# Performance work log

Hardware: AMD Instinct MI355X
Metric: run time of the kernel (lower is better)

Reference implementation:

```python
import jax, jax.numpy as jnp
import numpy as np

N = 100000   # nodes
E = 1600000  # edges
D = 64       # feature dim (input = hidden = output)
G = 256      # graphs in batch
EPS = 1e-5   # BatchNorm eps


def setup_inputs() -> dict:
    key = jax.random.key(0)
    ks = jax.random.split(key, 16)
    inp = {
        "x": jax.random.normal(ks[0], (N, D), dtype=jnp.float32),
        "edge_index": jax.random.randint(ks[1], (2, E), 0, N, dtype=jnp.int64),
        "batch": jnp.sort(jax.random.randint(ks[2], (N,), 0, G, dtype=jnp.int64)),
    }
    # GCNConv weights (glorot-ish) + biases, and BatchNorm affine params, 3 layers
    for i in range(3):
        inp[f"W{i+1}"] = jax.random.normal(ks[3 + i], (D, D), dtype=jnp.float32) / np.sqrt(D)
        inp[f"b{i+1}"] = jnp.zeros((D,), dtype=jnp.float32)
        inp[f"g{i+1}"] = jnp.ones((D,), dtype=jnp.float32)   # BN gamma
        inp[f"be{i+1}"] = jnp.zeros((D,), dtype=jnp.float32)  # BN beta
    return inp


def _batchnorm(x, gamma, beta):
    # BatchNorm1d in training mode: batch stats over the node dim (biased var)
    mean = jnp.mean(x, axis=0)
    var = jnp.mean(jnp.square(x - mean), axis=0)
    return (x - mean) * jax.lax.rsqrt(var + EPS) * gamma + beta


def reference(x, edge_index, batch, W1, b1, g1, be1, W2, b2, g2, be2, W3, b3, g3, be3):
    src, dst = edge_index[0], edge_index[1]
    # GCN normalization with self-loops: norm_ij = deg_i^-1/2 * deg_j^-1/2 over A + I
    loop = jnp.arange(N, dtype=src.dtype)
    src2 = jnp.concatenate([src, loop])
    dst2 = jnp.concatenate([dst, loop])
    deg = jax.ops.segment_sum(jnp.ones_like(src2, dtype=x.dtype), dst2, num_segments=N)
    dinv = jax.lax.rsqrt(deg)  # deg >= 1 thanks to self loops
    norm = (dinv[src2] * dinv[dst2])[:, None]  # [E+N, 1]

    def gcn_conv(h, W, b):
        h = h @ W                                   # [N, D] small GEMM
        msg = h[src2] * norm                        # per-edge gather (memory bound)
        return jax.ops.segment_sum(msg, dst2, num_segments=N) + b

    params = [(W1, b1, g1, be1), (W2, b2, g2, be2), (W3, b3, g3, be3)]
    h = x
    for i, (W, b, g, be) in enumerate(params):
        h = gcn_conv(h, W, b)
        h = _batchnorm(h, g, be)
        if i < 2:
            h = jax.nn.relu(h)
            # dropout(p=0.2) is identity in deterministic/eval reference

    # global mean + max pool per graph
    ones = jnp.ones((N,), dtype=h.dtype)
    cnt = jax.ops.segment_sum(ones, batch, num_segments=G)            # [G]
    s = jax.ops.segment_sum(h, batch, num_segments=G)                 # [G, D]
    mean = s / jnp.maximum(cnt, 1.0)[:, None]
    mx = jax.ops.segment_max(h, batch, num_segments=G)
    mx = jnp.where(cnt[:, None] > 0, mx, 0.0)
    return mean + mx
```

## Files before the change

kernel.cpp:

```cpp
#include <hip/hip_runtime.h>
#include <hip/hip_bf16.h>
#include <math.h>

#define N_NODES 100000
#define N_EDGES 1600000
#define DIM 64
#define N_GRAPHS 256
#define BN_EPS 1e-5f
#define N_XCD 8
#define BUCKET ((N_NODES + N_XCD - 1) / N_XCD)
#define FILL_CHUNKS 128
#define FILL_ESIZE ((N_EDGES + FILL_CHUNKS - 1) / FILL_CHUNKS)
#define CSR_STRIDE 48

__device__ inline unsigned short f2bf(float f) {
    __hip_bfloat16 h = __float2bfloat16(f);
    return *reinterpret_cast<unsigned short*>(&h);
}
__device__ inline unsigned int pack2bf(float a, float b) {
    return (unsigned int)f2bf(a) | ((unsigned int)f2bf(b) << 16);
}
__device__ inline float bf_lo(unsigned int u) { return __uint_as_float(u << 16); }
__device__ inline float bf_hi(unsigned int u) { return __uint_as_float(u & 0xffff0000u); }

__global__ __launch_bounds__(256) void hist_fused(const int* __restrict__ src,
                                                  const int* __restrict__ dst,
                                                  int* __restrict__ cnt,
                                                  int* __restrict__ csr_pad) {
    int chunk = blockIdx.x >> 3;
    int lo = (blockIdx.x & (N_XCD - 1)) * BUCKET;
    int e0 = chunk * FILL_ESIZE;
    int e1 = min(e0 + FILL_ESIZE, N_EDGES);
    for (int e = e0 + threadIdx.x; e < e1; e += 256) {
        int d = __builtin_nontemporal_load(&dst[e]);
        if ((unsigned)(d - lo) < (unsigned)BUCKET) {
            int r = atomicAdd(&cnt[d], 1);
            csr_pad[d * CSR_STRIDE + r] = __builtin_nontemporal_load(&src[e]);
        }
    }
}

__global__ void deg_fin(const int* __restrict__ cnt, float* __restrict__ dinv) {
    int i = blockIdx.x * blockDim.x + threadIdx.x;
    if (i < N_NODES) dinv[i] = rsqrtf((float)(cnt[i] + 1));
}

__global__ __launch_bounds__(256) void gemm_f32(const float* __restrict__ h,
                                                const float* __restrict__ W,
                                                const float* __restrict__ dinv,
                                                unsigned short* __restrict__ tb) {
    int tid = threadIdx.x;
    int d = tid & 63;
    int wv = tid >> 6;
    float wcol[64];
    #pragma unroll
    for (int k = 0; k < 64; ++k) wcol[k] = W[k * 64 + d];
    int nwaves = gridDim.x * 4;
    for (int row = blockIdx.x * 4 + wv; row < N_NODES; row += nwaves) {
        int urow = __builtin_amdgcn_readfirstlane(row);
        const float* hr = h + (size_t)urow * 64;
        float a0 = 0.f, a1 = 0.f, a2 = 0.f, a3 = 0.f;
        #pragma unroll
        for (int k = 0; k < 64; k += 4) {
            a0 = fmaf(hr[k + 0], wcol[k + 0], a0);
            a1 = fmaf(hr[k + 1], wcol[k + 1], a1);
            a2 = fmaf(hr[k + 2], wcol[k + 2], a2);
            a3 = fmaf(hr[k + 3], wcol[k + 3], a3);
        }
        float acc = (a0 + a1) + (a2 + a3);
        tb[(size_t)urow * 64 + d] = f2bf(acc * dinv[urow]);
    }
}

__global__ __launch_bounds__(256) void bnrelu(const unsigned short* __restrict__ agg,
                                              const float* __restrict__ stats,
                                              const float* __restrict__ gamma,
                                              const float* __restrict__ beta,
                                              float* __restrict__ hp) {
    __shared__ float scale[64], shift[64];
    int tid = threadIdx.x;
    if (tid < 64) {
        const float inv_n = 1.0f / (float)N_NODES;
        float mean = stats[tid] * inv_n;
        float var = fmaxf(stats[64 + tid] * inv_n - mean * mean, 0.f);
        float rs = rsqrtf(var + BN_EPS) * gamma[tid];
        scale[tid] = rs;
        shift[tid] = beta[tid] - mean * rs;
    }
    __syncthreads();
    const size_t total = (size_t)N_NODES * 8;
    for (size_t i = (size_t)blockIdx.x * 256 + tid; i < total; i += (size_t)gridDim.x * 256) {
        uint4 u = *reinterpret_cast<const uint4*>(agg + i * 8);
        int dd = (int)((i * 8) & 63);
        float4 o0, o1;
        o0.x = fmaxf(fmaf(bf_lo(u.x), scale[dd + 0], shift[dd + 0]), 0.f);
        o0.y = fmaxf(fmaf(bf_hi(u.x), scale[dd + 1], shift[dd + 1]), 0.f);
        o0.z = fmaxf(fmaf(bf_lo(u.y), scale[dd + 2], shift[dd + 2]), 0.f);
        o0.w = fmaxf(fmaf(bf_hi(u.y), scale[dd + 3], shift[dd + 3]), 0.f);
        o1.x = fmaxf(fmaf(bf_lo(u.z), scale[dd + 4], shift[dd + 4]), 0.f);
        o1.y = fmaxf(fmaf(bf_hi(u.z), scale[dd + 5], shift[dd + 5]), 0.f);
        o1.z = fmaxf(fmaf(bf_lo(u.w), scale[dd + 6], shift[dd + 6]), 0.f);
        o1.w = fmaxf(fmaf(bf_hi(u.w), scale[dd + 7], shift[dd + 7]), 0.f);
        *reinterpret_cast<float4*>(hp + i * 8) = o0;
        *reinterpret_cast<float4*>(hp + i * 8 + 4) = o1;
    }
}

__global__ __launch_bounds__(256) void gather_agg(const int* __restrict__ csr_pad,
                                                  const int* __restrict__ cnt,
                                                  const float* __restrict__ dinv,
                                                  const unsigned short* __restrict__ tb,
                                                  const float* __restrict__ bias,
                                                  unsigned short* __restrict__ out,
                                                  float* __restrict__ stats) {
    int tid = threadIdx.x;
    int wave = tid >> 6;
    int lane = tid & 63;
    int q    = lane >> 4;
    int ql   = lane & 15;

    float4 s4  = {0.f, 0.f, 0.f, 0.f};
    float4 sq4 = {0.f, 0.f, 0.f, 0.f};

    for (int v = blockIdx.x * 4 + wave; v < N_NODES; v += gridDim.x * 4) {
        int beg = v * CSR_STRIDE;
        int end = beg + cnt[v];
        float4 acc  = {0.f, 0.f, 0.f, 0.f};
        float4 acc2 = {0.f, 0.f, 0.f, 0.f};
        int e = beg + q;
        for (; e + 4 < end; e += 8) {
            int s0 = csr_pad[e];
            int s1 = csr_pad[e + 4];
            uint2 u0 = *reinterpret_cast<const uint2*>(tb + (size_t)s0 * 64 + ql * 4);
            uint2 u1 = *reinterpret_cast<const uint2*>(tb + (size_t)s1 * 64 + ql * 4);
            acc.x  += bf_lo(u0.x); acc.y  += bf_hi(u0.x);
            acc.z  += bf_lo(u0.y); acc.w  += bf_hi(u0.y);
            acc2.x += bf_lo(u1.x); acc2.y += bf_hi(u1.x);
            acc2.z += bf_lo(u1.y); acc2.w += bf_hi(u1.y);
        }
        if (e < end) {
            int s0 = csr_pad[e];
            uint2 u0 = *reinterpret_cast<const uint2*>(tb + (size_t)s0 * 64 + ql * 4);
            acc.x += bf_lo(u0.x); acc.y += bf_hi(u0.x);
            acc.z += bf_lo(u0.y); acc.w += bf_hi(u0.y);
        }
        acc.x += acc2.x; acc.y += acc2.y; acc.z += acc2.z; acc.w += acc2.w;

        acc.x += __shfl_xor(acc.x, 16, 64); acc.x += __shfl_xor(acc.x, 32, 64);
        acc.y += __shfl_xor(acc.y, 16, 64); acc.y += __shfl_xor(acc.y, 32, 64);
        acc.z += __shfl_xor(acc.z, 16, 64); acc.z += __shfl_xor(acc.z, 32, 64);
        acc.w += __shfl_xor(acc.w, 16, 64); acc.w += __shfl_xor(acc.w, 32, 64);

        if (q == 0) {
            float di = dinv[v];
            uint2 uv = *reinterpret_cast<const uint2*>(tb + (size_t)v * 64 + ql * 4);
            float4 bi = *reinterpret_cast<const float4*>(bias + ql * 4);
            float4 val;
            val.x = fmaf(di, acc.x + bf_lo(uv.x), bi.x);
            val.y = fmaf(di, acc.y + bf_hi(uv.x), bi.y);
            val.z = fmaf(di, acc.z + bf_lo(uv.y), bi.z);
            val.w = fmaf(di, acc.w + bf_hi(uv.y), bi.w);
            uint2 o;
            o.x = pack2bf(val.x, val.y);
            o.y = pack2bf(val.z, val.w);
            *reinterpret_cast<uint2*>(out + (size_t)v * 64 + ql * 4) = o;
            s4.x += val.x; s4.y += val.y; s4.z += val.z; s4.w += val.w;
            sq4.x += val.x * val.x; sq4.y += val.y * val.y;
            sq4.z += val.z * val.z; sq4.w += val.w * val.w;
        }
    }

    __shared__ float shs[4][64];
    __shared__ float shq[4][64];
    if (q == 0) {
        *reinterpret_cast<float4*>(&shs[wave][ql * 4]) = s4;
        *reinterpret_cast<float4*>(&shq[wave][ql * 4]) = sq4;
    }
    __syncthreads();
    if (tid < 64) {
        float S = shs[0][tid] + shs[1][tid] + shs[2][tid] + shs[3][tid];
        float Q = shq[0][tid] + shq[1][tid] + shq[2][tid] + shq[3][tid];
        unsafeAtomicAdd(&stats[tid], S);
        unsafeAtomicAdd(&stats[64 + tid], Q);
    }
}

__global__ __launch_bounds__(256) void pool_partial(const unsigned short* __restrict__ hb,
                                                    const int* __restrict__ batch,
                                                    const float* __restrict__ stats,
                                                    const float* __restrict__ gamma,
                                                    const float* __restrict__ beta,
                                                    float* __restrict__ pS,
                                                    float* __restrict__ pM) {
    int bid = blockIdx.x;
    int g = bid >> 2, p = bid & 3;
    __shared__ float scale[64], shift[64];
    __shared__ int bounds[2];
    int tid = threadIdx.x;
    if (tid < 64) {
        const float inv_n = 1.0f / (float)N_NODES;
        float mean = stats[tid] * inv_n;
        float var = fmaxf(stats[64 + tid] * inv_n - mean * mean, 0.f);
        float rs = rsqrtf(var + BN_EPS) * gamma[tid];
        scale[tid] = rs;
        shift[tid] = beta[tid] - mean * rs;
    }
    if (tid < 2) {
        int target = g + tid;
        int lo = 0, hi = N_NODES;
        while (lo < hi) {
            int mid = (lo + hi) >> 1;
            if (batch[mid] < target) lo = mid + 1; else hi = mid;
        }
        bounds[tid] = lo;
    }
    __syncthreads();
    int lo = bounds[0], hi = bounds[1];
    int d = tid & 63, g4 = tid >> 6;
    float sc = scale[d], sh = shift[d];
    float s = 0.f, m = -3.402823466e38f;
    for (int row = lo + p * 4 + g4; row < hi; row += 16) {
        float v = __uint_as_float(((unsigned int)hb[(size_t)row * 64 + d]) << 16);
        v = fmaf(v, sc, sh);
        s += v;
        m = fmaxf(m, v);
    }
    __shared__ float shs[8][64];
    shs[g4][d] = s;
    shs[4 + g4][d] = m;
    __syncthreads();
    if (tid < 64) {
        float S = shs[0][tid] + shs[1][tid] + shs[2][tid] + shs[3][tid];
        float M = fmaxf(fmaxf(shs[4][tid], shs[5][tid]), fmaxf(shs[6][tid], shs[7][tid]));
        pS[bid * 64 + tid] = S;
        pM[bid * 64 + tid] = M;
    }
}

__global__ __launch_bounds__(64) void pool_final(const int* __restrict__ batch,
                                                 const float* __restrict__ pS,
                                                 const float* __restrict__ pM,
                                                 float* __restrict__ out) {
    int g = blockIdx.x, d = threadIdx.x;
    __shared__ int bounds[2];
    if (d < 2) {
        int target = g + d;
        int lo = 0, hi = N_NODES;
        while (lo < hi) {
            int mid = (lo + hi) >> 1;
            if (batch[mid] < target) lo = mid + 1; else hi = mid;
        }
        bounds[d] = lo;
    }
    __syncthreads();
    int cnt = bounds[1] - bounds[0];
    int base = g * 4 * 64 + d;
    float S = (pS[base] + pS[base + 64]) + (pS[base + 128] + pS[base + 192]);
    float M = fmaxf(fmaxf(pM[base], pM[base + 64]), fmaxf(pM[base + 128], pM[base + 192]));
    float mean = S / fmaxf((float)cnt, 1.0f);
    out[g * 64 + d] = (cnt > 0) ? (mean + M) : 0.0f;
}

extern "C" void kernel_launch(void* const* d_in, const int* in_sizes, int n_in,
                              void* d_out, int out_size, void* d_ws, size_t ws_size,
                              hipStream_t stream) {
    const float* x     = (const float*)d_in[0];
    const int*   eidx  = (const int*)d_in[1];
    const int*   batch = (const int*)d_in[2];
    const float* W[3]  = {(const float*)d_in[3], (const float*)d_in[7],  (const float*)d_in[11]};
    const float* b[3]  = {(const float*)d_in[4], (const float*)d_in[8],  (const float*)d_in[12]};
    const float* gm[3] = {(const float*)d_in[5], (const float*)d_in[9],  (const float*)d_in[13]};
    const float* be[3] = {(const float*)d_in[6], (const float*)d_in[10], (const float*)d_in[14]};

    float*          hp    = (float*)d_ws;
    unsigned short* tb    = (unsigned short*)(hp + (size_t)N_NODES * 64);
    unsigned short* agg   = tb + (size_t)N_NODES * 64;
    float* dinv     = (float*)(agg + (size_t)N_NODES * 64);
    float* stats    = dinv + N_NODES;
    float* poolS    = stats + 384;
    float* poolM    = poolS + 1024 * 64;
    int*   cnt      = (int*)(poolM + 1024 * 64);
    int*   csr_pad  = cnt + N_NODES;

    const int* srcp = eidx;
    const int* dstp = eidx + N_EDGES;

    hipMemsetAsync(stats, 0, 384 * sizeof(float), stream);
    hipMemsetAsync(cnt, 0, N_NODES * sizeof(int), stream);

    hist_fused<<<FILL_CHUNKS * N_XCD, 256, 0, stream>>>(srcp, dstp, cnt, csr_pad);
    deg_fin<<<(N_NODES + 255) / 256, 256, 0, stream>>>(cnt, dinv);

    gemm_f32<<<1024, 256, 0, stream>>>(x, W[0], dinv, tb);
    gather_agg<<<2048, 256, 0, stream>>>(csr_pad, cnt, dinv, tb, b[0], agg, stats);

    bnrelu<<<1024, 256, 0, stream>>>(agg, stats, gm[0], be[0], hp);
    gemm_f32<<<1024, 256, 0, stream>>>(hp, W[1], dinv, tb);
    gather_agg<<<2048, 256, 0, stream>>>(csr_pad, cnt, dinv, tb, b[1], agg, stats + 128);

    bnrelu<<<1024, 256, 0, stream>>>(agg, stats + 128, gm[1], be[1], hp);
    gemm_f32<<<1024, 256, 0, stream>>>(hp, W[2], dinv, tb);
    gather_agg<<<2048, 256, 0, stream>>>(csr_pad, cnt, dinv, tb, b[2], agg, stats + 256);

    pool_partial<<<N_GRAPHS * 4, 256, 0, stream>>>(agg, batch, stats + 256, gm[2], be[2], poolS, poolM);
    pool_final<<<N_GRAPHS, 64, 0, stream>>>(batch, poolS, poolM, (float*)d_out);
}
```

Baseline: 473.4 us.

## Overlap edge histogram with first-layer GEMM in one kernel, apply dinv scaling afterwards

Merges the CSR histogram/fill and the first-layer x@W GEMM into a single launch: some blocks bucket edges while the others compute an unscaled bf16 product. A new finish_scale kernel then computes dinv from the counts and rescales the bf16 rows in place, replacing deg_fin. This removes a launch and lets the atomic-heavy histogram run alongside the compute-bound GEMM. The cost is an extra read-modify-write pass over the bf16 features and a second bf16 rounding of the scaled values.

```diff
diff --git a/kernel.cpp b/kernel.cpp
--- a/kernel.cpp
+++ b/kernel.cpp
@@ -12,6 +12,8 @@
 #define FILL_CHUNKS 128
 #define FILL_ESIZE ((N_EDGES + FILL_CHUNKS - 1) / FILL_CHUNKS)
 #define CSR_STRIDE 48
+#define HIST_BLOCKS (FILL_CHUNKS * N_XCD)
+#define GEMM0_BLOCKS 1024
 
 __device__ inline unsigned short f2bf(float f) {
     __hip_bfloat16 h = __float2bfloat16(f);
@@ -23,26 +25,67 @@
 __device__ inline float bf_lo(unsigned int u) { return __uint_as_float(u << 16); }
 __device__ inline float bf_hi(unsigned int u) { return __uint_as_float(u & 0xffff0000u); }
 
-__global__ __launch_bounds__(256) void hist_fused(const int* __restrict__ src,
+__global__ __launch_bounds__(256) void hist_gemm0(const int* __restrict__ src,
                                                   const int* __restrict__ dst,
                                                   int* __restrict__ cnt,
-                                                  int* __restrict__ csr_pad) {
-    int chunk = blockIdx.x >> 3;
-    int lo = (blockIdx.x & (N_XCD - 1)) * BUCKET;
-    int e0 = chunk * FILL_ESIZE;
-    int e1 = min(e0 + FILL_ESIZE, N_EDGES);
-    for (int e = e0 + threadIdx.x; e < e1; e += 256) {
-        int d = __builtin_nontemporal_load(&dst[e]);
-        if ((unsigned)(d - lo) < (unsigned)BUCKET) {
-            int r = atomicAdd(&cnt[d], 1);
-            csr_pad[d * CSR_STRIDE + r] = __builtin_nontemporal_load(&src[e]);
-        }
-    }
-}
-
-__global__ void deg_fin(const int* __restrict__ cnt, float* __restrict__ dinv) {
-    int i = blockIdx.x * blockDim.x + threadIdx.x;
-    if (i < N_NODES) dinv[i] = rsqrtf((float)(cnt[i] + 1));
+                                                  int* __restrict__ csr_pad,
+                                                  const float* __restrict__ x,
+                                                  const float* __restrict__ W,
+                                                  unsigned short* __restrict__ tb) {
+    if (blockIdx.x < HIST_BLOCKS) {
+        int chunk = blockIdx.x >> 3;
+        int lo = (blockIdx.x & (N_XCD - 1)) * BUCKET;
+        int e0 = chunk * FILL_ESIZE;
+        int e1 = min(e0 + FILL_ESIZE, N_EDGES);
+        for (int e = e0 + threadIdx.x; e < e1; e += 256) {
+            int d = __builtin_nontemporal_load(&dst[e]);
+            if ((unsigned)(d - lo) < (unsigned)BUCKET) {
+                int r = atomicAdd(&cnt[d], 1);
+                csr_pad[d * CSR_STRIDE + r] = __builtin_nontemporal_load(&src[e]);
+            }
+        }
+    } else {
+        int tid = threadIdx.x;
+        int d = tid & 63;
+        int wv = tid >> 6;
+        float wcol[64];
+        #pragma unroll
+        for (int k = 0; k < 64; ++k) wcol[k] = W[k * 64 + d];
+        int gb = blockIdx.x - HIST_BLOCKS;
+        int nwaves = GEMM0_BLOCKS * 4;
+        for (int row = gb * 4 + wv; row < N_NODES; row += nwaves) {
+            int urow = __builtin_amdgcn_readfirstlane(row);
+            const float* hr = x + (size_t)urow * 64;
+            float a0 = 0.f, a1 = 0.f, a2 = 0.f, a3 = 0.f;
+            #pragma unroll
+            for (int k = 0; k < 64; k += 4) {
+                a0 = fmaf(hr[k + 0], wcol[k + 0], a0);
+                a1 = fmaf(hr[k + 1], wcol[k + 1], a1);
+                a2 = fmaf(hr[k + 2], wcol[k + 2], a2);
+                a3 = fmaf(hr[k + 3], wcol[k + 3], a3);
+            }
+            float acc = (a0 + a1) + (a2 + a3);
+            tb[(size_t)urow * 64 + d] = f2bf(acc);
+        }
+    }
+}
+
+__global__ __launch_bounds__(256) void finish_scale(const int* __restrict__ cnt,
+                                                    unsigned short* __restrict__ tb,
+                                                    float* __restrict__ dinv) {
+    const int total = N_NODES * 8;
+    for (int i = blockIdx.x * 256 + threadIdx.x; i < total; i += gridDim.x * 256) {
+        int row = i >> 3;
+        float di = rsqrtf((float)(cnt[row] + 1));
+        uint4 u = *reinterpret_cast<const uint4*>(tb + (size_t)i * 8);
+        uint4 o;
+        o.x = pack2bf(bf_lo(u.x) * di, bf_hi(u.x) * di);
+        o.y = pack2bf(bf_lo(u.y) * di, bf_hi(u.y) * di);
+        o.z = pack2bf(bf_lo(u.z) * di, bf_hi(u.z) * di);
+        o.w = pack2bf(bf_lo(u.w) * di, bf_hi(u.w) * di);
+        *reinterpret_cast<uint4*>(tb + (size_t)i * 8) = o;
+        if ((i & 7) == 0) dinv[row] = di;
+    }
 }
 
 __global__ __launch_bounds__(256) void gemm_f32(const float* __restrict__ h,
@@ -288,10 +331,10 @@
     hipMemsetAsync(stats, 0, 384 * sizeof(float), stream);
     hipMemsetAsync(cnt, 0, N_NODES * sizeof(int), stream);
 
-    hist_fused<<<FILL_CHUNKS * N_XCD, 256, 0, stream>>>(srcp, dstp, cnt, csr_pad);
-    deg_fin<<<(N_NODES + 255) / 256, 256, 0, stream>>>(cnt, dinv);
-
-    gemm_f32<<<1024, 256, 0, stream>>>(x, W[0], dinv, tb);
+    hist_gemm0<<<HIST_BLOCKS + GEMM0_BLOCKS, 256, 0, stream>>>(srcp, dstp, cnt, csr_pad,
+                                                               x, W[0], tb);
+    finish_scale<<<1024, 256, 0, stream>>>(cnt, tb, dinv);
+
     gather_agg<<<2048, 256, 0, stream>>>(csr_pad, cnt, dinv, tb, b[0], agg, stats);
 
     bnrelu<<<1024, 256, 0, stream>>>(agg, stats, gm[0], be[0], hp);
```

Result: faster. 455.4 us (-3.8%).
